# Performance work log

Hardware: AMD Instinct MI355X
Metric: run time of the kernel (lower is better)

The kernel has to match this reference:

```python
import jax, jax.numpy as jnp
import numpy as np
from functools import partial

IMG, P, DIM, DEPTH, HEADS, MLP = 224, 16, 768, 6, 12, 3072
N = (IMG // P) ** 2            # 196 patches
PIX = P * P * 3                # 768 pixel values per patch
RATIO = 0.5
NUM_MASKED = int(RATIO * N)    # 98


def patchify(img):
    # b (h p1) (w p2) c -> b (h w) (p1 p2 c)
    b, H, W, c = img.shape
    g = H // P
    x = img.reshape(b, g, P, g, P, c)
    x = x.transpose(0, 1, 3, 2, 4, 5)
    return x.reshape(b, g * g, P * P * c)


def layernorm(x, s, b, eps=1e-5):
    m = jnp.mean(x, axis=-1, keepdims=True)
    v = jnp.var(x, axis=-1, keepdims=True)
    return (x - m) * jax.lax.rsqrt(v + eps) * s + b


def setup_inputs() -> dict:
    key = jax.random.key(0)
    ks = jax.random.split(key, 16)
    B = 64
    s = 0.02
    inp = {
        "img": jax.random.normal(ks[0], (B, IMG, IMG, 3), jnp.float32),
        "mask_noise": jax.random.uniform(ks[1], (B, N), jnp.float32),
        "patch_w": jax.random.normal(ks[2], (PIX, DIM), jnp.float32) * s,
        "patch_b": jnp.zeros((DIM,), jnp.float32),
        "pos_emb": jax.random.normal(ks[3], (1, N + 1, DIM), jnp.float32) * s,
        "mask_token": jax.random.normal(ks[4], (DIM,), jnp.float32),
        "ln1_s": jnp.ones((DEPTH, DIM), jnp.float32),
        "ln1_b": jnp.zeros((DEPTH, DIM), jnp.float32),
        "wqkv": jax.random.normal(ks[5], (DEPTH, DIM, 3 * DIM), jnp.float32) * s,
        "bqkv": jnp.zeros((DEPTH, 3 * DIM), jnp.float32),
        "wo": jax.random.normal(ks[6], (DEPTH, DIM, DIM), jnp.float32) * s,
        "bo": jnp.zeros((DEPTH, DIM), jnp.float32),
        "ln2_s": jnp.ones((DEPTH, DIM), jnp.float32),
        "ln2_b": jnp.zeros((DEPTH, DIM), jnp.float32),
        "w1": jax.random.normal(ks[7], (DEPTH, DIM, MLP), jnp.float32) * s,
        "b1": jnp.zeros((DEPTH, MLP), jnp.float32),
        "w2": jax.random.normal(ks[8], (DEPTH, MLP, DIM), jnp.float32) * s,
        "b2": jnp.zeros((DEPTH, DIM), jnp.float32),
        "pix_w": jax.random.normal(ks[9], (DIM, PIX), jnp.float32) * s,
        "pix_b": jnp.zeros((PIX,), jnp.float32),
    }
    return inp


def transformer(tokens, ln1_s, ln1_b, wqkv, bqkv, wo, bo, ln2_s, ln2_b, w1, b1, w2, b2):
    dh = DIM // HEADS
    scale = 1.0 / jnp.sqrt(jnp.float32(dh))

    def layer(x, p):
        l1s, l1b, Wqkv, Bqkv, Wo, Bo, l2s, l2b, W1, B1, W2, B2 = p
        h = layernorm(x, l1s, l1b)
        qkv = h @ Wqkv + Bqkv                              # [b,n,3D]
        b, n, _ = qkv.shape
        q, k, v = jnp.split(qkv.reshape(b, n, 3, HEADS, dh), 3, axis=2)
        q, k, v = (t[:, :, 0] for t in (q, k, v))          # [b,n,h,d]
        attn = jax.nn.softmax(jnp.einsum('bqhd,bkhd->bhqk', q, k) * scale, axis=-1)
        out = jnp.einsum('bhqk,bkhd->bqhd', attn, v).reshape(b, n, DIM)
        x = x + out @ Wo + Bo
        h = layernorm(x, l2s, l2b)
        x = x + jax.nn.gelu(h @ W1 + B1) @ W2 + B2
        return x, None

    params = (ln1_s, ln1_b, wqkv, bqkv, wo, bo, ln2_s, ln2_b, w1, b1, w2, b2)
    x, _ = jax.lax.scan(layer, tokens, params)
    return x


def reference(img, mask_noise, patch_w, patch_b, pos_emb, mask_token,
              ln1_s, ln1_b, wqkv, bqkv, wo, bo, ln2_s, ln2_b, w1, b1, w2, b2,
              pix_w, pix_b):
    patches = patchify(img)                               # [B,N,PIX]
    B = patches.shape[0]
    batch_range = jnp.arange(B)[:, None]
    pe = pos_emb[:, 1:N + 1]                              # skip cls position

    tokens = patches @ patch_w + patch_b + pe             # [B,N,D]
    mask_tokens = mask_token + pe                         # [1,N,D] broadcast

    _, masked_indices = jax.lax.top_k(mask_noise, NUM_MASKED)   # [B,K]
    bool_mask = jnp.zeros((B, N), bool).at[batch_range, masked_indices].set(True)
    tokens = jnp.where(bool_mask[..., None], mask_tokens, tokens)

    encoded = transformer(tokens, ln1_s, ln1_b, wqkv, bqkv, wo, bo,
                          ln2_s, ln2_b, w1, b1, w2, b2)

    encoded_mask = encoded[batch_range, masked_indices]   # [B,K,D]
    pred = encoded_mask @ pix_w + pix_b                   # [B,K,PIX]
    masked_patches = patches[batch_range, masked_indices]
    recon_loss = jnp.mean(jnp.abs(pred - masked_patches)) / NUM_MASKED
    return recon_loss
```

## Files before the change

kernel.cpp:

```cpp
#include <hip/hip_runtime.h>
#include <hip/hip_bf16.h>
#include <math.h>

#define BATCH   64
#define NPATCH  196
#define DIM     768
#define DEPTH   6
#define HEADS   12
#define DHEAD   64
#define MLPDIM  3072
#define NMASK   98
#define TOKENS  (BATCH*NPATCH)
#define MROWS   (BATCH*NMASK)
#define HALFROWS (TOKENS/2)

using bf16_t = __hip_bfloat16;
typedef short bf16x8 __attribute__((ext_vector_type(8)));
typedef short short4v __attribute__((ext_vector_type(4)));
typedef float floatx4 __attribute__((ext_vector_type(4)));

__device__ inline float gelu_f(float v) {
    const float c = 0.7978845608028654f;
    float t = tanhf(c * (v + 0.044715f * v * v * v));
    return 0.5f * v * (1.0f + t);
}

__device__ __forceinline__ short f2bf_s(float f) {
    bf16_t t = __float2bfloat16(f);
    return *reinterpret_cast<short*>(&t);
}

__device__ __forceinline__ void gload_lds16(const bf16_t* g, bf16_t* l) {
    __builtin_amdgcn_global_load_lds(
        (const __attribute__((address_space(1))) unsigned int*)g,
        (__attribute__((address_space(3))) unsigned int*)l, 16, 0, 0);
}

template<int MODE>
__global__ __launch_bounds__(256) void mm_bf16(
    const bf16_t* __restrict__ A, const bf16_t* __restrict__ BT,
    const float* __restrict__ bias, const float* __restrict__ Cin,
    void* __restrict__ Cout, int M, int N, int K)
{
    __shared__ __align__(16) bf16_t As[128 * 64];
    __shared__ __align__(16) bf16_t Bs[128 * 64];

    const int tid  = threadIdx.x;
    const int lane = tid & 63;
    const int wave = tid >> 6;
    const int wm = (wave >> 1) * 64;
    const int wn = (wave & 1) * 64;
    const int m0 = blockIdx.y * 128;
    const int n0 = blockIdx.x * 128;

    const int srow = tid >> 3;
    const int schunk = (tid & 7) ^ (srow & 7);
    const bf16_t* gA = A  + (size_t)(m0 + srow) * K + schunk * 8;
    const bf16_t* gB = BT + (size_t)(n0 + srow) * K + schunk * 8;
    bf16_t* lA = &As[tid * 8];
    bf16_t* lB = &Bs[tid * 8];

    floatx4 acc[4][4];
#pragma unroll
    for (int i = 0; i < 4; ++i)
#pragma unroll
        for (int j = 0; j < 4; ++j) acc[i][j] = (floatx4)0.0f;

    const int quad = lane >> 4;
    const int rm = lane & 15;

    for (int k0 = 0; k0 < K; k0 += 64) {
        __syncthreads();
#pragma unroll
        for (int i = 0; i < 4; ++i) {
            gload_lds16(gA + k0 + (size_t)(32 * i) * K, lA + i * 2048);
            gload_lds16(gB + k0 + (size_t)(32 * i) * K, lB + i * 2048);
        }
        __syncthreads();

#pragma unroll
        for (int kk = 0; kk < 2; ++kk) {
            const int kq = ((((kk << 2) | quad)) ^ (rm & 7)) * 8;
            bf16x8 a[4], b[4];
#pragma unroll
            for (int mi = 0; mi < 4; ++mi)
                a[mi] = *(const bf16x8*)&As[(wm + mi * 16 + rm) * 64 + kq];
#pragma unroll
            for (int ni = 0; ni < 4; ++ni)
                b[ni] = *(const bf16x8*)&Bs[(wn + ni * 16 + rm) * 64 + kq];
#pragma unroll
            for (int mi = 0; mi < 4; ++mi)
#pragma unroll
                for (int ni = 0; ni < 4; ++ni)
                    acc[mi][ni] = __builtin_amdgcn_mfma_f32_16x16x32_bf16(
                        a[mi], b[ni], acc[mi][ni], 0, 0, 0);
        }
    }

    const int cm = m0 + wm + quad * 4;
    const int cn = n0 + wn + rm;
#pragma unroll
    for (int mi = 0; mi < 4; ++mi) {
#pragma unroll
        for (int ni = 0; ni < 4; ++ni) {
#pragma unroll
            for (int r = 0; r < 4; ++r) {
                const int row = cm + mi * 16 + r;
                const int col = cn + ni * 16;
                float v = acc[mi][ni][r] + bias[col];
                const size_t idx = (size_t)row * N + col;
                if (MODE == 0) {
                    ((float*)Cout)[idx] = v;
                } else if (MODE == 1) {
                    ((bf16_t*)Cout)[idx] = __float2bfloat16(gelu_f(v));
                } else if (MODE == 2) {
                    ((float*)Cout)[idx] = v + Cin[idx];
                } else {
                    ((bf16_t*)Cout)[idx] = __float2bfloat16(v);
                }
            }
        }
    }
}

__global__ __launch_bounds__(256) void wconvT(
    const float* __restrict__ W, bf16_t* __restrict__ WT, int K, int N)
{
    __shared__ float t[32][33];
    const size_t off = (size_t)blockIdx.z * K * N;
    const int k0 = blockIdx.y * 32, n0 = blockIdx.x * 32;
    const int r = threadIdx.x >> 5, c = threadIdx.x & 31;
#pragma unroll
    for (int i = 0; i < 4; ++i)
        t[r + i * 8][c] = W[off + (size_t)(k0 + r + i * 8) * N + n0 + c];
    __syncthreads();
#pragma unroll
    for (int i = 0; i < 4; ++i)
        WT[off + (size_t)(n0 + r + i * 8) * K + k0 + c] =
            __float2bfloat16(t[c][r + i * 8]);
}

__global__ __launch_bounds__(256) void patchify_kernel(
    const float* __restrict__ img, bf16_t* __restrict__ patches)
{
    const int row = blockIdx.x;
    const int b = row / NPATCH, p = row % NPATCH;
    const int gy = p / 14, gx = p % 14;
    for (int e = threadIdx.x; e < 768; e += 256) {
        const int c = e % 3, pix = e / 3;
        const int py = pix / 16, px = pix % 16;
        const size_t src = (((size_t)b * 224 + gy * 16 + py) * 224 + gx * 16 + px) * 3 + c;
        patches[(size_t)row * 768 + e] = __float2bfloat16(img[src]);
    }
}

__global__ __launch_bounds__(256) void mask_kernel(
    const float* __restrict__ noise, int* __restrict__ flags, int* __restrict__ midx)
{
    const int b = blockIdx.x;
    __shared__ float v[NPATCH];
    const int t = threadIdx.x;
    if (t < NPATCH) v[t] = noise[b * NPATCH + t];
    __syncthreads();
    if (t < NPATCH) {
        const float mine = v[t];
        int r = 0;
        for (int j = 0; j < NPATCH; ++j) {
            const float o = v[j];
            r += (o > mine) || (o == mine && j < t);
        }
        const int f = (r < NMASK) ? 1 : 0;
        flags[b * NPATCH + t] = f;
        if (f) midx[b * NMASK + r] = t;
    }
}

__global__ __launch_bounds__(256) void pe_mask_kernel(
    float* __restrict__ x, const float* __restrict__ pos_emb,
    const float* __restrict__ mask_token, const int* __restrict__ flags)
{
    const int wave = threadIdx.x >> 6, lane = threadIdx.x & 63;
    const int row = blockIdx.x * 4 + wave;
    const int n = row % NPATCH;
    const int masked = flags[row];
    const float* pe = pos_emb + (size_t)(n + 1) * 768;
    float* xr = x + (size_t)row * 768;
#pragma unroll
    for (int j = 0; j < 3; ++j) {
        const int off = j * 256 + lane * 4;
        const float4 pev = *(const float4*)(pe + off);
        float4 o;
        if (masked) {
            const float4 mt = *(const float4*)(mask_token + off);
            o.x = mt.x + pev.x; o.y = mt.y + pev.y;
            o.z = mt.z + pev.z; o.w = mt.w + pev.w;
        } else {
            const float4 xv = *(const float4*)(xr + off);
            o.x = xv.x + pev.x; o.y = xv.y + pev.y;
            o.z = xv.z + pev.z; o.w = xv.w + pev.w;
        }
        *(float4*)(xr + off) = o;
    }
}

__global__ __launch_bounds__(256) void ln_kernel(
    const float* __restrict__ x, bf16_t* __restrict__ out,
    const float* __restrict__ s, const float* __restrict__ bvec)
{
    const int wave = threadIdx.x >> 6, lane = threadIdx.x & 63;
    const int row = blockIdx.x * 4 + wave;
    const float* xr = x + (size_t)row * 768;

    float4 v[3];
    float sum = 0.0f, sq = 0.0f;
#pragma unroll
    for (int j = 0; j < 3; ++j) {
        v[j] = *(const float4*)(xr + j * 256 + lane * 4);
        sum += v[j].x + v[j].y + v[j].z + v[j].w;
        sq  += v[j].x * v[j].x + v[j].y * v[j].y + v[j].z * v[j].z + v[j].w * v[j].w;
    }
#pragma unroll
    for (int off = 32; off; off >>= 1) {
        sum += __shfl_xor(sum, off, 64);
        sq  += __shfl_xor(sq, off, 64);
    }
    const float mean = sum * (1.0f / 768.0f);
    const float var = sq * (1.0f / 768.0f) - mean * mean;
    const float inv = rsqrtf(var + 1e-5f);

    bf16_t* orow = out + (size_t)row * 768;
#pragma unroll
    for (int j = 0; j < 3; ++j) {
        const int off = j * 256 + lane * 4;
        const float4 sv = *(const float4*)(s + off);
        const float4 bv = *(const float4*)(bvec + off);
        short4v o;
        o[0] = f2bf_s((v[j].x - mean) * inv * sv.x + bv.x);
        o[1] = f2bf_s((v[j].y - mean) * inv * sv.y + bv.y);
        o[2] = f2bf_s((v[j].z - mean) * inv * sv.z + bv.z);
        o[3] = f2bf_s((v[j].w - mean) * inv * sv.w + bv.w);
        *(short4v*)(orow + off) = o;
    }
}

__global__ __launch_bounds__(256) void attn_kernel(
    const bf16_t* __restrict__ qkv, bf16_t* __restrict__ out)
{
    const int bh = blockIdx.x;
    const int b = bh / HEADS, h = bh % HEADS;
    const int tid = threadIdx.x, lane = tid & 63, wave = tid >> 6;
    const int quad = lane >> 4, l16 = lane & 15;
    const int wq = wave * 64;

    __shared__ __align__(16) short Vt[64][68];
    __shared__ __align__(16) short Plds[4][64][68];
    __shared__ float red[4][64];

    const size_t tok0 = (size_t)b * NPATCH;
    const int hoff = h * 64;

    bf16x8 qf[4][2];
#pragma unroll
    for (int ni = 0; ni < 4; ++ni) {
        const int q = wq + ni * 16 + l16;
        const int qe = q < 195 ? q : 195;
#pragma unroll
        for (int ks = 0; ks < 2; ++ks)
            qf[ni][ks] = *(const bf16x8*)(qkv + (tok0 + qe) * 2304 + hoff + ks * 32 + quad * 8);
    }

    floatx4 accO[4][4];
#pragma unroll
    for (int i = 0; i < 4; ++i)
#pragma unroll
        for (int j = 0; j < 4; ++j) accO[i][j] = (floatx4)0.0f;
    float mrun[4], lrun[4];
#pragma unroll
    for (int ni = 0; ni < 4; ++ni) { mrun[ni] = -1e30f; lrun[ni] = 0.0f; }

    for (int kc = 0; kc < 256; kc += 64) {
        __syncthreads();
        {
            const int kl = tid & 63;
            const int dg = tid >> 6;
            const int key = kc + kl;
            if (key < NPATCH) {
                const bf16_t* src = qkv + (tok0 + key) * 2304 + 1536 + hoff + dg * 16;
                bf16x8 v0 = *(const bf16x8*)src;
                bf16x8 v1 = *(const bf16x8*)(src + 8);
#pragma unroll
                for (int j = 0; j < 8; ++j) {
                    Vt[dg * 16 + j][kl]     = v0[j];
                    Vt[dg * 16 + 8 + j][kl] = v1[j];
                }
            } else {
#pragma unroll
                for (int j = 0; j < 16; ++j) Vt[dg * 16 + j][kl] = 0;
            }
        }
        __syncthreads();

        bf16x8 af[4][2];
#pragma unroll
        for (int mi = 0; mi < 4; ++mi) {
            const int key = kc + mi * 16 + l16;
            const int ke = key < 195 ? key : 195;
#pragma unroll
            for (int ks = 0; ks < 2; ++ks)
                af[mi][ks] = *(const bf16x8*)(qkv + (tok0 + ke) * 2304 + 768 + hoff + ks * 32 + quad * 8);
        }
        floatx4 accS[4][4];
#pragma unroll
        for (int i = 0; i < 4; ++i)
#pragma unroll
            for (int j = 0; j < 4; ++j) accS[i][j] = (floatx4)0.0f;
#pragma unroll
        for (int mi = 0; mi < 4; ++mi)
#pragma unroll
            for (int ni = 0; ni < 4; ++ni)
#pragma unroll
                for (int ks = 0; ks < 2; ++ks)
                    accS[mi][ni] = __builtin_amdgcn_mfma_f32_16x16x32_bf16(
                        af[mi][ks], qf[ni][ks], accS[mi][ni], 0, 0, 0);

#pragma unroll
        for (int mi = 0; mi < 4; ++mi) {
#pragma unroll
            for (int r = 0; r < 4; ++r) {
                const int key = kc + mi * 16 + quad * 4 + r;
                const bool valid = key < NPATCH;
#pragma unroll
                for (int ni = 0; ni < 4; ++ni)
                    accS[mi][ni][r] = valid ? accS[mi][ni][r] * 0.125f : -1e30f;
            }
        }

        float alpha[4];
#pragma unroll
        for (int ni = 0; ni < 4; ++ni) {
            float mx = -1e30f;
#pragma unroll
            for (int mi = 0; mi < 4; ++mi)
#pragma unroll
                for (int r = 0; r < 4; ++r) mx = fmaxf(mx, accS[mi][ni][r]);
            mx = fmaxf(mx, __shfl_xor(mx, 16, 64));
            mx = fmaxf(mx, __shfl_xor(mx, 32, 64));
            const float mnew = fmaxf(mrun[ni], mx);
            float s = 0.0f;
#pragma unroll
            for (int mi = 0; mi < 4; ++mi)
#pragma unroll
                for (int r = 0; r < 4; ++r) {
                    const float p = __expf(accS[mi][ni][r] - mnew);
                    accS[mi][ni][r] = p;
                    s += p;
                }
            s += __shfl_xor(s, 16, 64);
            s += __shfl_xor(s, 32, 64);
            alpha[ni] = __expf(mrun[ni] - mnew);
            lrun[ni] = lrun[ni] * alpha[ni] + s;
            mrun[ni] = mnew;
        }
        if (quad == 0) {
#pragma unroll
            for (int ni = 0; ni < 4; ++ni) red[wave][ni * 16 + l16] = alpha[ni];
        }

#pragma unroll
        for (int mi = 0; mi < 4; ++mi)
#pragma unroll
            for (int ni = 0; ni < 4; ++ni) {
                short4v pk;
#pragma unroll
                for (int r = 0; r < 4; ++r) pk[r] = f2bf_s(accS[mi][ni][r]);
                *(short4v*)&Plds[wave][ni * 16 + l16][mi * 16 + quad * 4] = pk;
            }
        asm volatile("s_waitcnt lgkmcnt(0)" ::: "memory");

#pragma unroll
        for (int mi = 0; mi < 4; ++mi) {
            const float4 al = *(const float4*)&red[wave][mi * 16 + quad * 4];
#pragma unroll
            for (int ni = 0; ni < 4; ++ni) {
                accO[mi][ni][0] *= al.x;
                accO[mi][ni][1] *= al.y;
                accO[mi][ni][2] *= al.z;
                accO[mi][ni][3] *= al.w;
            }
        }

#pragma unroll
        for (int ks = 0; ks < 2; ++ks) {
            bf16x8 pa[4], vb[4];
#pragma unroll
            for (int mi = 0; mi < 4; ++mi) {
                short4v lo = *(const short4v*)&Plds[wave][mi * 16 + l16][ks * 32 + quad * 8];
                short4v hi = *(const short4v*)&Plds[wave][mi * 16 + l16][ks * 32 + quad * 8 + 4];
                pa[mi] = __builtin_shufflevector(lo, hi, 0, 1, 2, 3, 4, 5, 6, 7);
            }
#pragma unroll
            for (int ni = 0; ni < 4; ++ni) {
                short4v lo = *(const short4v*)&Vt[ni * 16 + l16][ks * 32 + quad * 8];
                short4v hi = *(const short4v*)&Vt[ni * 16 + l16][ks * 32 + quad * 8 + 4];
                vb[ni] = __builtin_shufflevector(lo, hi, 0, 1, 2, 3, 4, 5, 6, 7);
            }
#pragma unroll
            for (int mi = 0; mi < 4; ++mi)
#pragma unroll
                for (int ni = 0; ni < 4; ++ni)
                    accO[mi][ni] = __builtin_amdgcn_mfma_f32_16x16x32_bf16(
                        pa[mi], vb[ni], accO[mi][ni], 0, 0, 0);
        }
    }

    if (quad == 0) {
#pragma unroll
        for (int ni = 0; ni < 4; ++ni) red[wave][ni * 16 + l16] = lrun[ni];
    }
    asm volatile("s_waitcnt lgkmcnt(0)" ::: "memory");
#pragma unroll
    for (int mi = 0; mi < 4; ++mi) {
        const float4 lv = *(const float4*)&red[wave][mi * 16 + quad * 4];
        const float inv[4] = {1.0f / lv.x, 1.0f / lv.y, 1.0f / lv.z, 1.0f / lv.w};
#pragma unroll
        for (int r = 0; r < 4; ++r) {
            const int q = wq + mi * 16 + quad * 4 + r;
            if (q < NPATCH) {
#pragma unroll
                for (int ni = 0; ni < 4; ++ni) {
                    const int d = ni * 16 + l16;
                    out[(tok0 + q) * 768 + hoff + d] =
                        __float2bfloat16(accO[mi][ni][r] * inv[r]);
                }
            }
        }
    }
}

__global__ __launch_bounds__(256) void gather_kernel(
    const float* __restrict__ x, const int* __restrict__ midx, bf16_t* __restrict__ em)
{
    const int row = blockIdx.x;
    const int b = row / NMASK;
    const int n = midx[row];
    const float* src = x + (size_t)(b * NPATCH + n) * 768;
    bf16_t* dst = em + (size_t)row * 768;
    for (int e = threadIdx.x; e < 768; e += 256) dst[e] = __float2bfloat16(src[e]);
}

__global__ void zero_kernel(float* __restrict__ p) {
    if (threadIdx.x == 0 && blockIdx.x == 0) p[0] = 0.0f;
}

__global__ __launch_bounds__(256) void loss_kernel(
    const float* __restrict__ pred, const float* __restrict__ img,
    const int* __restrict__ midx, float* __restrict__ acc)
{
    const size_t total = (size_t)MROWS * 768;
    float part = 0.0f;
    for (size_t idx = (size_t)blockIdx.x * blockDim.x + threadIdx.x; idx < total;
         idx += (size_t)gridDim.x * blockDim.x) {
        const int e = (int)(idx % 768);
        const int row = (int)(idx / 768);
        const int b = row / NMASK;
        const int n = midx[row];
        const int c = e % 3, pix = e / 3;
        const int py = pix / 16, px = pix % 16;
        const int gy = n / 14, gx = n % 14;
        const float ref =
            img[(((size_t)b * 224 + gy * 16 + py) * 224 + gx * 16 + px) * 3 + c];
        part += fabsf(pred[idx] - ref);
    }
#pragma unroll
    for (int off = 32; off; off >>= 1) part += __shfl_down(part, off, 64);
    __shared__ float sp[4];
    if ((threadIdx.x & 63) == 0) sp[threadIdx.x >> 6] = part;
    __syncthreads();
    if (threadIdx.x == 0) atomicAdd(acc, sp[0] + sp[1] + sp[2] + sp[3]);
}

__global__ void finalize_kernel(const float* __restrict__ acc, float* __restrict__ out)
{
    if (threadIdx.x == 0 && blockIdx.x == 0)
        out[0] = acc[0] * (float)(1.0 / 472055808.0);
}

extern "C" void kernel_launch(void* const* d_in, const int* in_sizes, int n_in,
                              void* d_out, int out_size, void* d_ws, size_t ws_size,
                              hipStream_t stream)
{
    const float* img      = (const float*)d_in[0];
    const float* noise    = (const float*)d_in[1];
    const float* patch_w  = (const float*)d_in[2];
    const float* patch_b  = (const float*)d_in[3];
    const float* pos_emb  = (const float*)d_in[4];
    const float* mask_tok = (const float*)d_in[5];
    const float* ln1_s    = (const float*)d_in[6];
    const float* ln1_b    = (const float*)d_in[7];
    const float* wqkv     = (const float*)d_in[8];
    const float* bqkv     = (const float*)d_in[9];
    const float* wo       = (const float*)d_in[10];
    const float* bo       = (const float*)d_in[11];
    const float* ln2_s    = (const float*)d_in[12];
    const float* ln2_b    = (const float*)d_in[13];
    const float* w1       = (const float*)d_in[14];
    const float* b1       = (const float*)d_in[15];
    const float* w2       = (const float*)d_in[16];
    const float* b2       = (const float*)d_in[17];
    const float* pix_w    = (const float*)d_in[18];
    const float* pix_b    = (const float*)d_in[19];

    const size_t TOK = (size_t)TOKENS * 768;
    float*  x    = (float*)d_ws;
    bf16_t* h    = (bf16_t*)(x + TOK);
    bf16_t* qbuf = h + TOK;
    bf16_t* wts  = qbuf + (size_t)TOKENS * 2304;
    size_t o = 0;
    bf16_t* patch_wT = wts + o; o += (size_t)768 * 768;
    bf16_t* wqkvT    = wts + o; o += (size_t)DEPTH * 2304 * 768;
    bf16_t* woT      = wts + o; o += (size_t)DEPTH * 768 * 768;
    bf16_t* w1T      = wts + o; o += (size_t)DEPTH * 3072 * 768;
    bf16_t* w2T      = wts + o; o += (size_t)DEPTH * 768 * 3072;
    bf16_t* pix_wT   = wts + o; o += (size_t)768 * 768;
    int* flags = (int*)(wts + o);
    int* midx  = flags + TOKENS;
    float* acc = (float*)(midx + MROWS);

    bf16_t* patches = qbuf;
    float*  pred    = (float*)qbuf;

    wconvT<<<dim3(768/32, 768/32, 1), 256, 0, stream>>>(patch_w, patch_wT, 768, 768);
    wconvT<<<dim3(2304/32, 768/32, DEPTH), 256, 0, stream>>>(wqkv, wqkvT, 768, 2304);
    wconvT<<<dim3(768/32, 768/32, DEPTH), 256, 0, stream>>>(wo, woT, 768, 768);
    wconvT<<<dim3(3072/32, 768/32, DEPTH), 256, 0, stream>>>(w1, w1T, 768, 3072);
    wconvT<<<dim3(768/32, 3072/32, DEPTH), 256, 0, stream>>>(w2, w2T, 3072, 768);
    wconvT<<<dim3(768/32, 768/32, 1), 256, 0, stream>>>(pix_w, pix_wT, 768, 768);

    patchify_kernel<<<TOKENS, 256, 0, stream>>>(img, patches);
    mask_kernel<<<BATCH, 256, 0, stream>>>(noise, flags, midx);

    mm_bf16<0><<<dim3(768/128, TOKENS/128), 256, 0, stream>>>(
        patches, patch_wT, patch_b, nullptr, x, TOKENS, 768, 768);
    pe_mask_kernel<<<TOKENS/4, 256, 0, stream>>>(x, pos_emb, mask_tok, flags);

    for (int l = 0; l < DEPTH; ++l) {
        ln_kernel<<<TOKENS/4, 256, 0, stream>>>(x, h, ln1_s + l * 768, ln1_b + l * 768);
        mm_bf16<3><<<dim3(2304/128, TOKENS/128), 256, 0, stream>>>(
            h, wqkvT + (size_t)l * 2304 * 768, bqkv + l * 2304, nullptr, qbuf,
            TOKENS, 2304, 768);
        attn_kernel<<<BATCH * HEADS, 256, 0, stream>>>(qbuf, h);
        mm_bf16<2><<<dim3(768/128, TOKENS/128), 256, 0, stream>>>(
            h, woT + (size_t)l * 768 * 768, bo + l * 768, x, x, TOKENS, 768, 768);
        ln_kernel<<<TOKENS/4, 256, 0, stream>>>(x, h, ln2_s + l * 768, ln2_b + l * 768);
        for (int ch = 0; ch < 2; ++ch) {
            bf16_t* hA = h + (size_t)ch * HALFROWS * 768;
            float*  xC = x + (size_t)ch * HALFROWS * 768;
            mm_bf16<1><<<dim3(MLPDIM/128, HALFROWS/128), 256, 0, stream>>>(
                hA, w1T + (size_t)l * 3072 * 768, b1 + l * MLPDIM, nullptr, qbuf,
                HALFROWS, MLPDIM, 768);
            mm_bf16<2><<<dim3(768/128, HALFROWS/128), 256, 0, stream>>>(
                qbuf, w2T + (size_t)l * 768 * 3072, b2 + l * 768, xC, xC,
                HALFROWS, 768, MLPDIM);
        }
    }

    gather_kernel<<<MROWS, 256, 0, stream>>>(x, midx, h);
    mm_bf16<0><<<dim3(768/128, MROWS/128), 256, 0, stream>>>(
        h, pix_wT, pix_b, nullptr, pred, MROWS, 768, 768);

    zero_kernel<<<1, 64, 0, stream>>>(acc);
    loss_kernel<<<4704, 256, 0, stream>>>(pred, img, midx, acc);
    finalize_kernel<<<1, 64, 0, stream>>>(acc, (float*)d_out);
}
```

Measured before the change: 2.858 ms.

## Double-buffer GEMM LDS tiles, remap workgroups per XCD, unchunk MLP when workspace allows

The bf16 GEMM kernel now keeps two LDS buffers and issues the global-to-LDS loads for the next K tile before running MFMAs on the current one. This removes one barrier per iteration and hides load latency behind compute. Workgroup IDs are remapped so that consecutive tiles land on the same XCD, which should improve L2 reuse. The MLP is run as one full-token pass when the workspace can hold the full intermediate, which cuts kernel launches. In exchange, LDS use per block doubles to 64KB, which may lower occupancy.

```diff
diff --git a/kernel.cpp b/kernel.cpp
--- a/kernel.cpp
+++ b/kernel.cpp
@@ -42,23 +42,29 @@
     const float* __restrict__ bias, const float* __restrict__ Cin,
     void* __restrict__ Cout, int M, int N, int K)
 {
-    __shared__ __align__(16) bf16_t As[128 * 64];
-    __shared__ __align__(16) bf16_t Bs[128 * 64];
+    __shared__ __align__(16) bf16_t As[2][128 * 64];
+    __shared__ __align__(16) bf16_t Bs[2][128 * 64];
 
     const int tid  = threadIdx.x;
     const int lane = tid & 63;
     const int wave = tid >> 6;
     const int wm = (wave >> 1) * 64;
     const int wn = (wave & 1) * 64;
-    const int m0 = blockIdx.y * 128;
-    const int n0 = blockIdx.x * 128;
+
+    const int gx  = gridDim.x;
+    const int nwg = gx * gridDim.y;
+    const int orig = blockIdx.y * gx + blockIdx.x;
+    const int qq = nwg >> 3, rr = nwg & 7;
+    const int xcd = orig & 7, seq = orig >> 3;
+    const int wg = (xcd < rr ? xcd * (qq + 1) : rr * (qq + 1) + (xcd - rr) * qq) + seq;
+    const int m0 = (wg / gx) * 128;
+    const int n0 = (wg % gx) * 128;
 
     const int srow = tid >> 3;
     const int schunk = (tid & 7) ^ (srow & 7);
     const bf16_t* gA = A  + (size_t)(m0 + srow) * K + schunk * 8;
     const bf16_t* gB = BT + (size_t)(n0 + srow) * K + schunk * 8;
-    bf16_t* lA = &As[tid * 8];
-    bf16_t* lB = &Bs[tid * 8];
+    const int lds_off = tid * 8;
 
     floatx4 acc[4][4];
 #pragma unroll
@@ -68,32 +74,55 @@
 
     const int quad = lane >> 4;
     const int rm = lane & 15;
-
-    for (int k0 = 0; k0 < K; k0 += 64) {
-        __syncthreads();
-#pragma unroll
-        for (int i = 0; i < 4; ++i) {
-            gload_lds16(gA + k0 + (size_t)(32 * i) * K, lA + i * 2048);
-            gload_lds16(gB + k0 + (size_t)(32 * i) * K, lB + i * 2048);
-        }
-        __syncthreads();
+    const int nt = K >> 6;
+
+#pragma unroll
+    for (int i = 0; i < 4; ++i) {
+        gload_lds16(gA + (size_t)(32 * i) * K, &As[0][lds_off] + i * 2048);
+        gload_lds16(gB + (size_t)(32 * i) * K, &Bs[0][lds_off] + i * 2048);
+    }
+    asm volatile("s_waitcnt vmcnt(0)" ::: "memory");
+    __builtin_amdgcn_s_barrier();
+    asm volatile("" ::: "memory");
+
+    int cur = 0;
+    for (int t = 0; t < nt; ++t) {
+        const bf16_t* sA = cur ? &As[1][0] : &As[0][0];
+        const bf16_t* sB = cur ? &Bs[1][0] : &Bs[0][0];
+        if (t + 1 < nt) {
+            bf16_t* dA = cur ? &As[0][lds_off] : &As[1][lds_off];
+            bf16_t* dB = cur ? &Bs[0][lds_off] : &Bs[1][lds_off];
+            const int koff = (t + 1) * 64;
+#pragma unroll
+            for (int i = 0; i < 4; ++i) {
+                gload_lds16(gA + koff + (size_t)(32 * i) * K, dA + i * 2048);
+                gload_lds16(gB + koff + (size_t)(32 * i) * K, dB + i * 2048);
+            }
+        }
 
 #pragma unroll
         for (int kk = 0; kk < 2; ++kk) {
-            const int kq = ((((kk << 2) | quad)) ^ (rm & 7)) * 8;
+            const int kq = (((kk << 2) | quad) ^ (rm & 7)) * 8;
             bf16x8 a[4], b[4];
 #pragma unroll
             for (int mi = 0; mi < 4; ++mi)
-                a[mi] = *(const bf16x8*)&As[(wm + mi * 16 + rm) * 64 + kq];
+                a[mi] = *(const bf16x8*)&sA[(wm + mi * 16 + rm) * 64 + kq];
 #pragma unroll
             for (int ni = 0; ni < 4; ++ni)
-                b[ni] = *(const bf16x8*)&Bs[(wn + ni * 16 + rm) * 64 + kq];
+                b[ni] = *(const bf16x8*)&sB[(wn + ni * 16 + rm) * 64 + kq];
 #pragma unroll
             for (int mi = 0; mi < 4; ++mi)
 #pragma unroll
                 for (int ni = 0; ni < 4; ++ni)
                     acc[mi][ni] = __builtin_amdgcn_mfma_f32_16x16x32_bf16(
                         a[mi], b[ni], acc[mi][ni], 0, 0, 0);
+        }
+
+        if (t + 1 < nt) {
+            asm volatile("s_waitcnt vmcnt(0)" ::: "memory");
+            __builtin_amdgcn_s_barrier();
+            asm volatile("" ::: "memory");
+            cur ^= 1;
         }
     }
 
@@ -526,6 +555,12 @@
     int* midx  = flags + TOKENS;
     float* acc = (float*)(midx + MROWS);
 
+    size_t used = (size_t)((char*)(acc + 1) - (char*)d_ws);
+    used = (used + 255) & ~(size_t)255;
+    bf16_t* mlpbuf = (bf16_t*)((char*)d_ws + used);
+    const bool fullmlp =
+        ws_size >= used + (size_t)TOKENS * MLPDIM * sizeof(bf16_t);
+
     bf16_t* patches = qbuf;
     float*  pred    = (float*)qbuf;
 
@@ -552,15 +587,24 @@
         mm_bf16<2><<<dim3(768/128, TOKENS/128), 256, 0, stream>>>(
             h, woT + (size_t)l * 768 * 768, bo + l * 768, x, x, TOKENS, 768, 768);
         ln_kernel<<<TOKENS/4, 256, 0, stream>>>(x, h, ln2_s + l * 768, ln2_b + l * 768);
-        for (int ch = 0; ch < 2; ++ch) {
-            bf16_t* hA = h + (size_t)ch * HALFROWS * 768;
-            float*  xC = x + (size_t)ch * HALFROWS * 768;
-            mm_bf16<1><<<dim3(MLPDIM/128, HALFROWS/128), 256, 0, stream>>>(
-                hA, w1T + (size_t)l * 3072 * 768, b1 + l * MLPDIM, nullptr, qbuf,
-                HALFROWS, MLPDIM, 768);
-            mm_bf16<2><<<dim3(768/128, HALFROWS/128), 256, 0, stream>>>(
-                qbuf, w2T + (size_t)l * 768 * 3072, b2 + l * 768, xC, xC,
-                HALFROWS, 768, MLPDIM);
+        if (fullmlp) {
+            mm_bf16<1><<<dim3(MLPDIM/128, TOKENS/128), 256, 0, stream>>>(
+                h, w1T + (size_t)l * 3072 * 768, b1 + l * MLPDIM, nullptr, mlpbuf,
+                TOKENS, MLPDIM, 768);
+            mm_bf16<2><<<dim3(768/128, TOKENS/128), 256, 0, stream>>>(
+                mlpbuf, w2T + (size_t)l * 768 * 3072, b2 + l * 768, x, x,
+                TOKENS, 768, MLPDIM);
+        } else {
+            for (int ch = 0; ch < 2; ++ch) {
+                bf16_t* hA = h + (size_t)ch * HALFROWS * 768;
+                float*  xC = x + (size_t)ch * HALFROWS * 768;
+                mm_bf16<1><<<dim3(MLPDIM/128, HALFROWS/128), 256, 0, stream>>>(
+                    hA, w1T + (size_t)l * 3072 * 768, b1 + l * MLPDIM, nullptr, qbuf,
+                    HALFROWS, MLPDIM, 768);
+                mm_bf16<2><<<dim3(768/128, HALFROWS/128), 256, 0, stream>>>(
+                    qbuf, w2T + (size_t)l * 768 * 3072, b2 + l * 768, xC, xC,
+                    HALFROWS, 768, MLPDIM);
+            }
         }
     }
 
```

New measurement: 2.990 ms. +4.6%, slower.

## Add 64x64-tile GEMM for N=768 outputs and XCD-aware block swizzle

Applied to the files above, without the earlier changes.

Adds a 64x64-tile variant of the bf16 MFMA GEMM and uses it for the GEMMs whose output width is 768 (patch embed, attention out-proj, MLP down-proj, pixel head). The aim is more workgroups on the 256-CU GPU, since the 128x128 tiling gave only about 588 blocks for these shapes. It also adds a remap of workgroup IDs across the 8 XCDs so that neighbouring tiles share an XCD's L2. The smaller tiles give less operand reuse per byte loaded from LDS and global memory, and twice as many k-loop barriers per unit of work.

```diff
diff --git a/kernel.cpp b/kernel.cpp
--- a/kernel.cpp
+++ b/kernel.cpp
@@ -36,6 +36,12 @@
         (__attribute__((address_space(3))) unsigned int*)l, 16, 0, 0);
 }
 
+__device__ __forceinline__ int xcd_swz(int orig, int nwg) {
+    const int qq = nwg >> 3, rr = nwg & 7;
+    const int xcd = orig & 7, seq = orig >> 3;
+    return (xcd < rr ? xcd * (qq + 1) : rr * (qq + 1) + (xcd - rr) * qq) + seq;
+}
+
 template<int MODE>
 __global__ __launch_bounds__(256) void mm_bf16(
     const bf16_t* __restrict__ A, const bf16_t* __restrict__ BT,
@@ -50,8 +56,11 @@
     const int wave = tid >> 6;
     const int wm = (wave >> 1) * 64;
     const int wn = (wave & 1) * 64;
-    const int m0 = blockIdx.y * 128;
-    const int n0 = blockIdx.x * 128;
+
+    const int gx  = gridDim.x;
+    const int wg = xcd_swz(blockIdx.y * gx + blockIdx.x, gx * gridDim.y);
+    const int m0 = (wg / gx) * 128;
+    const int n0 = (wg % gx) * 128;
 
     const int srow = tid >> 3;
     const int schunk = (tid & 7) ^ (srow & 7);
@@ -80,7 +89,7 @@
 
 #pragma unroll
         for (int kk = 0; kk < 2; ++kk) {
-            const int kq = ((((kk << 2) | quad)) ^ (rm & 7)) * 8;
+            const int kq = (((kk << 2) | quad) ^ (rm & 7)) * 8;
             bf16x8 a[4], b[4];
 #pragma unroll
             for (int mi = 0; mi < 4; ++mi)
@@ -103,6 +112,96 @@
     for (int mi = 0; mi < 4; ++mi) {
 #pragma unroll
         for (int ni = 0; ni < 4; ++ni) {
+#pragma unroll
+            for (int r = 0; r < 4; ++r) {
+                const int row = cm + mi * 16 + r;
+                const int col = cn + ni * 16;
+                float v = acc[mi][ni][r] + bias[col];
+                const size_t idx = (size_t)row * N + col;
+                if (MODE == 0) {
+                    ((float*)Cout)[idx] = v;
+                } else if (MODE == 1) {
+                    ((bf16_t*)Cout)[idx] = __float2bfloat16(gelu_f(v));
+                } else if (MODE == 2) {
+                    ((float*)Cout)[idx] = v + Cin[idx];
+                } else {
+                    ((bf16_t*)Cout)[idx] = __float2bfloat16(v);
+                }
+            }
+        }
+    }
+}
+
+template<int MODE>
+__global__ __launch_bounds__(256) void mm64_bf16(
+    const bf16_t* __restrict__ A, const bf16_t* __restrict__ BT,
+    const float* __restrict__ bias, const float* __restrict__ Cin,
+    void* __restrict__ Cout, int M, int N, int K)
+{
+    __shared__ __align__(16) bf16_t As[64 * 64];
+    __shared__ __align__(16) bf16_t Bs[64 * 64];
+
+    const int tid  = threadIdx.x;
+    const int lane = tid & 63;
+    const int wave = tid >> 6;
+    const int wm = (wave >> 1) * 32;
+    const int wn = (wave & 1) * 32;
+
+    const int gx  = gridDim.x;
+    const int wg = xcd_swz(blockIdx.y * gx + blockIdx.x, gx * gridDim.y);
+    const int m0 = (wg / gx) * 64;
+    const int n0 = (wg % gx) * 64;
+
+    const int srow = tid >> 3;
+    const int schunk = (tid & 7) ^ (srow & 7);
+    const bf16_t* gA = A  + (size_t)(m0 + srow) * K + schunk * 8;
+    const bf16_t* gB = BT + (size_t)(n0 + srow) * K + schunk * 8;
+    bf16_t* lA = &As[tid * 8];
+    bf16_t* lB = &Bs[tid * 8];
+
+    floatx4 acc[2][2];
+#pragma unroll
+    for (int i = 0; i < 2; ++i)
+#pragma unroll
+        for (int j = 0; j < 2; ++j) acc[i][j] = (floatx4)0.0f;
+
+    const int quad = lane >> 4;
+    const int rm = lane & 15;
+
+    for (int k0 = 0; k0 < K; k0 += 64) {
+        __syncthreads();
+#pragma unroll
+        for (int i = 0; i < 2; ++i) {
+            gload_lds16(gA + k0 + (size_t)(32 * i) * K, lA + i * 2048);
+            gload_lds16(gB + k0 + (size_t)(32 * i) * K, lB + i * 2048);
+        }
+        __syncthreads();
+
+#pragma unroll
+        for (int kk = 0; kk < 2; ++kk) {
+            const int kq = (((kk << 2) | quad) ^ (rm & 7)) * 8;
+            bf16x8 a[2], b[2];
+#pragma unroll
+            for (int mi = 0; mi < 2; ++mi)
+                a[mi] = *(const bf16x8*)&As[(wm + mi * 16 + rm) * 64 + kq];
+#pragma unroll
+            for (int ni = 0; ni < 2; ++ni)
+                b[ni] = *(const bf16x8*)&Bs[(wn + ni * 16 + rm) * 64 + kq];
+#pragma unroll
+            for (int mi = 0; mi < 2; ++mi)
+#pragma unroll
+                for (int ni = 0; ni < 2; ++ni)
+                    acc[mi][ni] = __builtin_amdgcn_mfma_f32_16x16x32_bf16(
+                        a[mi], b[ni], acc[mi][ni], 0, 0, 0);
+        }
+    }
+
+    const int cm = m0 + wm + quad * 4;
+    const int cn = n0 + wn + rm;
+#pragma unroll
+    for (int mi = 0; mi < 2; ++mi) {
+#pragma unroll
+        for (int ni = 0; ni < 2; ++ni) {
 #pragma unroll
             for (int r = 0; r < 4; ++r) {
                 const int row = cm + mi * 16 + r;
@@ -539,7 +638,7 @@
     patchify_kernel<<<TOKENS, 256, 0, stream>>>(img, patches);
     mask_kernel<<<BATCH, 256, 0, stream>>>(noise, flags, midx);
 
-    mm_bf16<0><<<dim3(768/128, TOKENS/128), 256, 0, stream>>>(
+    mm64_bf16<0><<<dim3(768/64, TOKENS/64), 256, 0, stream>>>(
         patches, patch_wT, patch_b, nullptr, x, TOKENS, 768, 768);
     pe_mask_kernel<<<TOKENS/4, 256, 0, stream>>>(x, pos_emb, mask_tok, flags);
 
@@ -549,7 +648,7 @@
             h, wqkvT + (size_t)l * 2304 * 768, bqkv + l * 2304, nullptr, qbuf,
             TOKENS, 2304, 768);
         attn_kernel<<<BATCH * HEADS, 256, 0, stream>>>(qbuf, h);
-        mm_bf16<2><<<dim3(768/128, TOKENS/128), 256, 0, stream>>>(
+        mm64_bf16<2><<<dim3(768/64, TOKENS/64), 256, 0, stream>>>(
             h, woT + (size_t)l * 768 * 768, bo + l * 768, x, x, TOKENS, 768, 768);
         ln_kernel<<<TOKENS/4, 256, 0, stream>>>(x, h, ln2_s + l * 768, ln2_b + l * 768);
         for (int ch = 0; ch < 2; ++ch) {
@@ -558,14 +657,14 @@
             mm_bf16<1><<<dim3(MLPDIM/128, HALFROWS/128), 256, 0, stream>>>(
                 hA, w1T + (size_t)l * 3072 * 768, b1 + l * MLPDIM, nullptr, qbuf,
                 HALFROWS, MLPDIM, 768);
-            mm_bf16<2><<<dim3(768/128, HALFROWS/128), 256, 0, stream>>>(
+            mm64_bf16<2><<<dim3(768/64, HALFROWS/64), 256, 0, stream>>>(
                 qbuf, w2T + (size_t)l * 768 * 3072, b2 + l * 768, xC, xC,
                 HALFROWS, 768, MLPDIM);
         }
     }
 
     gather_kernel<<<MROWS, 256, 0, stream>>>(x, midx, h);
-    mm_bf16<0><<<dim3(768/128, MROWS/128), 256, 0, stream>>>(
+    mm64_bf16<0><<<dim3(768/64, MROWS/64), 256, 0, stream>>>(
         h, pix_wT, pix_b, nullptr, pred, MROWS, 768, 768);
 
     zero_kernel<<<1, 64, 0, stream>>>(acc);
```

Result: faster. 2.556 ms (-10.6%).
